# Kernel optimization log

Hardware: AMD Instinct MI355X
Metric: run time of the kernel (lower is better)

Reference implementation:

```python
import jax, jax.numpy as jnp
import numpy as np

B, S, D, H = 1, 4096, 1024, 16
DH = D // H  # 64
SCALE = D ** 0.5  # original divides by input_dim**0.5, not head_dim**0.5


def setup_inputs() -> dict:
    key = jax.random.key(0)
    ks = jax.random.split(key, 11)
    s = lambda i, shape, sc=1.0: jax.random.normal(ks[i], shape, dtype=jnp.float32) * sc
    w_init = 1.0 / np.sqrt(D)
    return {
        "q": s(0, (B, S, D)),
        "k": s(1, (B, S, D)),
        "v": s(2, (B, S, D)),
        "Wq": s(3, (H, D, DH), w_init),
        "bq": jnp.zeros((H, DH), jnp.float32),
        "Wk": s(4, (H, D, DH), w_init),
        "bk": jnp.zeros((H, DH), jnp.float32),
        "Wv": s(5, (H, D, DH), w_init),
        "bv": jnp.zeros((H, DH), jnp.float32),
        "Wo": s(6, (D, D), w_init),
        "bo": jnp.zeros((D,), jnp.float32),
    }


def reference(q, k, v, Wq, bq, Wk, bk, Wv, bv, Wo, bo):
    # Per-head Dense projections, batched over heads: [B,S,D] x [H,D,dh] -> [B,H,S,dh]
    Q = jnp.einsum("bsd,hde->bhse", q, Wq) + bq[None, :, None, :]
    K = jnp.einsum("bsd,hde->bhse", k, Wk) + bk[None, :, None, :]
    V = jnp.einsum("bsd,hde->bhse", v, Wv) + bv[None, :, None, :]
    # Scaled dot-product attention; note scale = sqrt(input_dim) as in source
    scores = jnp.einsum("bhse,bhte->bhst", Q, K) / SCALE  # [B,H,S,S]
    attn = jax.nn.softmax(scores, axis=-1)
    out = jnp.einsum("bhst,bhte->bhse", attn, V)  # [B,H,S,dh]
    # Concat heads along feature dim (head order matches the Python loop)
    concat = out.transpose(0, 2, 1, 3).reshape(q.shape[0], q.shape[1], H * DH)
    return concat @ Wo + bo
```

## Files before the change

### kernel.cpp

```cpp
#include <hip/hip_runtime.h>
#include <hip/hip_bf16.h>

#define S_LEN 4096
#define D_MODEL 1024
#define NH 16
#define DHEAD 64
#define QSCALE 0.0450843293f

typedef __attribute__((ext_vector_type(8))) short short8;
typedef __attribute__((ext_vector_type(4))) float floatx4;

__device__ __forceinline__ unsigned short f2bf(float f) {
    unsigned int x = __float_as_uint(f);
    x += 0x7fffu + ((x >> 16) & 1u);
    return (unsigned short)(x >> 16);
}

__device__ __forceinline__ float exp2_fast(float x) {
    return __builtin_amdgcn_exp2f(x);
}

__device__ __forceinline__ void async_copy16(const unsigned short* g, unsigned short* l) {
    __builtin_amdgcn_global_load_lds(
        (const __attribute__((address_space(1))) void*)g,
        (__attribute__((address_space(3))) void*)l, 16, 0, 0);
}

__global__ __launch_bounds__(256) void prep_all(
    const float* __restrict__ q, const float* __restrict__ k,
    const float* __restrict__ v,
    const float* __restrict__ Wq, const float* __restrict__ Wk,
    const float* __restrict__ Wv, const float* __restrict__ Wo,
    unsigned short* __restrict__ dst, unsigned short* __restrict__ ws)
{
    __shared__ float L[64][65];
    const int tid = threadIdx.x;

    if (blockIdx.x < 6144) {
        long i = (long)(blockIdx.x * 256 + tid) * 8;
        int which = (int)(i >> 22);
        long off = i & ((1 << 22) - 1);
        const float* src = (which == 0) ? q : (which == 1) ? k : v;
        float4 f0 = *(const float4*)&src[off];
        float4 f1 = *(const float4*)&src[off + 4];
        uint4 o;
        o.x = (unsigned int)f2bf(f0.x) | ((unsigned int)f2bf(f0.y) << 16);
        o.y = (unsigned int)f2bf(f0.z) | ((unsigned int)f2bf(f0.w) << 16);
        o.z = (unsigned int)f2bf(f1.x) | ((unsigned int)f2bf(f1.y) << 16);
        o.w = (unsigned int)f2bf(f1.z) | ((unsigned int)f2bf(f1.w) << 16);
        *(uint4*)&dst[i] = o;
        return;
    }

    const int bx  = blockIdx.x - 6144;
    const int mat = bx >> 8;

    if (mat < 3) {
        const float* W = (mat == 0) ? Wq : (mat == 1) ? Wk : Wv;
        unsigned short* WT = ws + (size_t)mat * (1u << 20);
        int h  = (bx >> 4) & 15;
        int dt = bx & 15;
        #pragma unroll
        for (int i = 0; i < 16; i++) {
            int idx = i * 256 + tid;
            int dp = idx >> 6, e = idx & 63;
            L[e][dp] = W[h * 65536 + (dt * 64 + dp) * 64 + e];
        }
        __syncthreads();
        #pragma unroll
        for (int i = 0; i < 16; i++) {
            int idx = i * 256 + tid;
            int e = idx >> 6, dp = idx & 63;
            WT[(h * 64 + e) * 1024 + dt * 64 + dp] = f2bf(L[e][dp]);
        }
    } else {
        unsigned short* WoT = ws + (size_t)3 * (1u << 20);
        int rt = (bx >> 4) & 15;
        int ct = bx & 15;
        #pragma unroll
        for (int i = 0; i < 16; i++) {
            int idx = i * 256 + tid;
            int dp = idx >> 6, np = idx & 63;
            L[np][dp] = Wo[(rt * 64 + dp) * 1024 + ct * 64 + np];
        }
        __syncthreads();
        #pragma unroll
        for (int i = 0; i < 16; i++) {
            int idx = i * 256 + tid;
            int np = idx >> 6, dp = idx & 63;
            WoT[(ct * 64 + np) * 1024 + rt * 64 + dp] = f2bf(L[np][dp]);
        }
    }
}

#define GEMM_CORE(XPTR, WPTR)                                                   \
    _Pragma("unroll")                                                           \
    for (int i = 0; i < 4; i++) {                                               \
        async_copy16(&XPTR[(size_t)(m0 + srow + i * 8) * D_MODEL + scol],       \
                     &LB[(wave * 32 + i * 8) * 64]);                            \
        async_copy16(&WPTR[(size_t)(n0 + srow + i * 8) * D_MODEL + scol],       \
                     &LB[16384 + (wave * 32 + i * 8) * 64]);                    \
    }                                                                           \
    asm volatile("s_waitcnt vmcnt(0)" ::: "memory");                            \
    __builtin_amdgcn_s_barrier();                                               \
    for (int k0 = 0; k0 < D_MODEL; k0 += 64) {                                  \
        const int cb = (k0 >> 6) & 1;                                           \
        const unsigned short* Ac = LB + cb * 8192;                              \
        const unsigned short* Bc = LB + 16384 + cb * 8192;                      \
        if (k0 + 64 < D_MODEL) {                                                \
            unsigned short* An = LB + (cb ^ 1) * 8192;                          \
            unsigned short* Bn = LB + 16384 + (cb ^ 1) * 8192;                  \
            _Pragma("unroll")                                                   \
            for (int i = 0; i < 4; i++) {                                       \
                async_copy16(&XPTR[(size_t)(m0 + srow + i * 8) * D_MODEL + k0 + 64 + scol], \
                             &An[(wave * 32 + i * 8) * 64]);                    \
                async_copy16(&WPTR[(size_t)(n0 + srow + i * 8) * D_MODEL + k0 + 64 + scol], \
                             &Bn[(wave * 32 + i * 8) * 64]);                    \
            }                                                                   \
        }                                                                       \
        _Pragma("unroll")                                                       \
        for (int ks = 0; ks < 2; ks++) {                                        \
            short8 af[4], bf[4];                                                \
            _Pragma("unroll")                                                   \
            for (int i = 0; i < 4; i++)                                         \
                af[i] = *(const short8*)&Ac[(wr * 64 + i * 16 + m) * 64 + ks * 32 + quad * 8]; \
            _Pragma("unroll")                                                   \
            for (int j = 0; j < 4; j++)                                         \
                bf[j] = *(const short8*)&Bc[(wc * 64 + j * 16 + m) * 64 + ks * 32 + quad * 8]; \
            __builtin_amdgcn_s_setprio(1);                                      \
            _Pragma("unroll")                                                   \
            for (int i = 0; i < 4; i++) {                                       \
                _Pragma("unroll")                                               \
                for (int j = 0; j < 4; j++)                                     \
                    acc[i][j] = __builtin_amdgcn_mfma_f32_16x16x32_bf16(af[i], bf[j], acc[i][j], 0, 0, 0); \
            }                                                                   \
            __builtin_amdgcn_s_setprio(0);                                      \
        }                                                                       \
        asm volatile("s_waitcnt vmcnt(0)" ::: "memory");                        \
        __builtin_amdgcn_s_barrier();                                           \
    }

__global__ __launch_bounds__(256) void qkv_gemm(
    const unsigned short* __restrict__ Xbase, const unsigned short* __restrict__ WTbase,
    const float* __restrict__ bq, const float* __restrict__ bk,
    const float* __restrict__ bv,
    unsigned short* __restrict__ Qbuf, unsigned short* __restrict__ Kbuf,
    unsigned short* __restrict__ Vbuf)
{
    __shared__ __align__(16) unsigned short LB[32768];

    const int z = blockIdx.z;
    const unsigned short* X  = Xbase + (size_t)z * (4u << 20);
    const unsigned short* WT = WTbase + (size_t)z * (1u << 20);
    const float* bias = (z == 0) ? bq : (z == 1) ? bk : bv;

    const int n0 = blockIdx.x * 128;
    const int m0 = blockIdx.y * 128;
    const int tid = threadIdx.x, wave = tid >> 6, lane = tid & 63;
    const int m = lane & 15, quad = lane >> 4;
    const int wr = wave >> 1, wc = wave & 1;
    const int srow = wave * 32 + (lane >> 3);
    const int scol = (lane & 7) * 8;

    floatx4 acc[4][4];
    #pragma unroll
    for (int i = 0; i < 4; i++)
        #pragma unroll
        for (int j = 0; j < 4; j++) acc[i][j] = (floatx4){0.f, 0.f, 0.f, 0.f};

    GEMM_CORE(X, WT)

    if (z == 2) {
        #pragma unroll
        for (int j = 0; j < 4; j++) {
            int n = n0 + wc * 64 + j * 16 + m;
            int h = n >> 6, e = n & 63;
            float bvv = bias[n];
            #pragma unroll
            for (int i = 0; i < 4; i++) {
                int sbase = m0 + wr * 64 + i * 16 + quad * 4;
                ushort4 pk;
                pk.x = f2bf(acc[i][j][0] + bvv);
                pk.y = f2bf(acc[i][j][1] + bvv);
                pk.z = f2bf(acc[i][j][2] + bvv);
                pk.w = f2bf(acc[i][j][3] + bvv);
                *(ushort4*)&Vbuf[h * (DHEAD * S_LEN) + e * S_LEN + sbase] = pk;
            }
        }
        return;
    }

    const float scale = (z == 0) ? QSCALE : 1.0f;
    unsigned short* outp = (z == 0) ? Qbuf : Kbuf;
    __syncthreads();
    unsigned short* stage = LB + (wc ? 8192 : 0);
    #pragma unroll
    for (int j = 0; j < 4; j++) {
        int e = j * 16 + m;
        float bvv = bias[n0 + wc * 64 + e];
        #pragma unroll
        for (int i = 0; i < 4; i++) {
            int rbase = wr * 64 + i * 16 + quad * 4;
            #pragma unroll
            for (int r = 0; r < 4; r++) {
                int rowl = rbase + r;
                stage[rowl * 64 + (e ^ ((rowl & 7) << 3))] =
                    f2bf((acc[i][j][r] + bvv) * scale);
            }
        }
    }
    __syncthreads();
    const int h0 = n0 >> 6;
    const size_t base0 = (size_t)h0 * (S_LEN * DHEAD) + (size_t)m0 * DHEAD;
    const size_t base1 = base0 + (size_t)(S_LEN * DHEAD);
    #pragma unroll
    for (int s = 0; s < 4; s++) {
        int o = tid * 8 + s * 2048;
        int row = o >> 6, c0 = o & 63;
        int cs = c0 ^ ((row & 7) << 3);
        *(uint4*)&outp[base0 + o] = *(const uint4*)&LB[row * 64 + cs];
        *(uint4*)&outp[base1 + o] = *(const uint4*)&LB[8192 + row * 64 + cs];
    }
}

__global__ __launch_bounds__(256) void out_gemm(
    const unsigned short* __restrict__ Cbuf, const unsigned short* __restrict__ WoT,
    const float* __restrict__ bo, float* __restrict__ out)
{
    __shared__ __align__(16) unsigned short LB[32768];

    const int n0 = blockIdx.x * 128;
    const int m0 = blockIdx.y * 128;
    const int tid = threadIdx.x, wave = tid >> 6, lane = tid & 63;
    const int m = lane & 15, quad = lane >> 4;
    const int wr = wave >> 1, wc = wave & 1;
    const int srow = wave * 32 + (lane >> 3);
    const int scol = (lane & 7) * 8;

    floatx4 acc[4][4];
    #pragma unroll
    for (int i = 0; i < 4; i++)
        #pragma unroll
        for (int j = 0; j < 4; j++) acc[i][j] = (floatx4){0.f, 0.f, 0.f, 0.f};

    GEMM_CORE(Cbuf, WoT)

    __syncthreads();
    float* Fs = (float*)LB;
    #pragma unroll
    for (int half = 0; half < 2; half++) {
        if (wr == half) {
            #pragma unroll
            for (int j = 0; j < 4; j++) {
                int c = wc * 64 + j * 16 + m;
                float bvv = bo[n0 + c];
                #pragma unroll
                for (int i = 0; i < 4; i++) {
                    int rbase = i * 16 + quad * 4;
                    #pragma unroll
                    for (int r = 0; r < 4; r++) {
                        int rowl = rbase + r;
                        Fs[rowl * 128 + (c ^ ((rowl & 7) << 2))] = acc[i][j][r] + bvv;
                    }
                }
            }
        }
        __syncthreads();
        #pragma unroll
        for (int s = 0; s < 8; s++) {
            int o = tid * 4 + s * 1024;
            int row = o >> 7, c0 = o & 127;
            int cs = c0 ^ ((row & 7) << 2);
            *(float4*)&out[(size_t)(m0 + half * 64 + row) * D_MODEL + n0 + c0] =
                *(const float4*)&Fs[row * 128 + cs];
        }
        __syncthreads();
    }
}

__global__ __launch_bounds__(512) void attn_kernel(
    const unsigned short* __restrict__ Q, const unsigned short* __restrict__ K,
    const unsigned short* __restrict__ VT, unsigned short* __restrict__ concat)
{
    __shared__ __align__(16) unsigned char ldsraw[65536];
    unsigned short* lds16 = (unsigned short*)ldsraw;

    const int h  = blockIdx.y;
    const int q0 = blockIdx.x * 256;
    const unsigned short* Qh = Q  + h * (S_LEN * DHEAD);
    const unsigned short* Kh = K  + h * (S_LEN * DHEAD);
    const unsigned short* Vh = VT + h * (DHEAD * S_LEN);

    const int tid  = threadIdx.x;
    const int wave = tid >> 6;
    const int wt   = wave & 3;
    const int wq2  = wave >> 2;
    const int lane = tid & 63;
    const int m    = lane & 15;
    const int quad = lane >> 4;
    const int swz  = (m & 7) << 3;
    const int lrow = lane >> 3;
    const int lcol = ((lane & 7) * 8) ^ (lrow << 3);

    unsigned short* Ps = lds16 + 16384;

    #pragma unroll
    for (int i = 0; i < 4; i++) {
        int c = 4 * wave + i;
        async_copy16(&Qh[(size_t)(q0 + 8 * c + lrow) * DHEAD + lcol], Ps + c * 512);
    }
    async_copy16(&Kh[(size_t)(8 * wave + lrow) * DHEAD + lcol], lds16 + wave * 512);
    async_copy16(&Vh[(size_t)(8 * wave + lrow) * S_LEN + lcol], lds16 + 8192 + wave * 512);
    asm volatile("s_waitcnt vmcnt(0)" ::: "memory");
    __builtin_amdgcn_s_barrier();

    short8 bq[8][2];
    #pragma unroll
    for (int qc = 0; qc < 8; qc++)
        #pragma unroll
        for (int ks = 0; ks < 2; ks++)
            bq[qc][ks] = *(const short8*)&Ps[(wq2 * 128 + qc * 16 + m) * 64 + ((ks * 32 + quad * 8) ^ swz)];
    __syncthreads();

    short8 vone;
    #pragma unroll
    for (int i = 0; i < 8; i++) vone[i] = (short)0x3F80;

    floatx4 O[2][4];
    #pragma unroll
    for (int mi = 0; mi < 2; mi++)
        #pragma unroll
        for (int nb = 0; nb < 4; nb++) O[mi][nb] = (floatx4){0.f, 0.f, 0.f, 0.f};
    floatx4 Lacc[2];
    Lacc[0] = (floatx4){0.f, 0.f, 0.f, 0.f};
    Lacc[1] = (floatx4){0.f, 0.f, 0.f, 0.f};

    for (int t0 = 0; t0 < S_LEN; t0 += 64) {
        const int cur = (t0 >> 6) & 1;
        unsigned short* Ksc = lds16 + cur * 4096;
        unsigned short* Vsc = lds16 + 8192 + cur * 4096;

        if (t0) {
            asm volatile("s_waitcnt vmcnt(0)" ::: "memory");
            __builtin_amdgcn_s_barrier();
        }
        if (t0 + 64 < S_LEN) {
            unsigned short* Ksn = lds16 + (cur ^ 1) * 4096;
            unsigned short* Vsn = lds16 + 8192 + (cur ^ 1) * 4096;
            async_copy16(&Kh[(size_t)(t0 + 64 + 8 * wave + lrow) * DHEAD + lcol],
                         Ksn + wave * 512);
            async_copy16(&Vh[(size_t)(8 * wave + lrow) * S_LEN + t0 + 64 + lcol],
                         Vsn + wave * 512);
        }

        floatx4 st[8];
        #pragma unroll
        for (int qc = 0; qc < 8; qc++) st[qc] = (floatx4){0.f, 0.f, 0.f, 0.f};
        #pragma unroll
        for (int ks = 0; ks < 2; ks++) {
            short8 a = *(const short8*)&Ksc[(wt * 16 + m) * 64 + ((ks * 32 + quad * 8) ^ swz)];
            __builtin_amdgcn_s_setprio(1);
            #pragma unroll
            for (int qc = 0; qc < 8; qc++)
                st[qc] = __builtin_amdgcn_mfma_f32_16x16x32_bf16(a, bq[qc][ks], st[qc], 0, 0, 0);
            __builtin_amdgcn_s_setprio(0);
        }

        #pragma unroll
        for (int qc = 0; qc < 8; qc++) {
            float p0 = exp2_fast(st[qc][0]);
            float p1 = exp2_fast(st[qc][1]);
            float p2 = exp2_fast(st[qc][2]);
            float p3 = exp2_fast(st[qc][3]);
            unsigned r0, r1;
            asm("v_cvt_pk_bf16_f32 %0, %1, %2" : "=v"(r0) : "v"(p0), "v"(p1));
            asm("v_cvt_pk_bf16_f32 %0, %1, %2" : "=v"(r1) : "v"(p2), "v"(p3));
            uint2 pk;
            pk.x = r0;
            pk.y = r1;
            *(uint2*)&Ps[(wq2 * 128 + qc * 16 + m) * 64 + ((wt * 16 + quad * 4) ^ swz)] = pk;
        }
        asm volatile("s_waitcnt lgkmcnt(0)" ::: "memory");
        __builtin_amdgcn_s_barrier();

        #pragma unroll
        for (int ks = 0; ks < 2; ks++) {
            short8 ap0 = *(const short8*)&Ps[(wave * 32 + m) * 64 + ((ks * 32 + quad * 8) ^ swz)];
            short8 ap1 = *(const short8*)&Ps[(wave * 32 + 16 + m) * 64 + ((ks * 32 + quad * 8) ^ swz)];
            __builtin_amdgcn_s_setprio(1);
            #pragma unroll
            for (int nb = 0; nb < 4; nb++) {
                short8 bv = *(const short8*)&Vsc[(nb * 16 + m) * 64 + ((ks * 32 + quad * 8) ^ swz)];
                O[0][nb] = __builtin_amdgcn_mfma_f32_16x16x32_bf16(ap0, bv, O[0][nb], 0, 0, 0);
                O[1][nb] = __builtin_amdgcn_mfma_f32_16x16x32_bf16(ap1, bv, O[1][nb], 0, 0, 0);
            }
            Lacc[0] = __builtin_amdgcn_mfma_f32_16x16x32_bf16(ap0, vone, Lacc[0], 0, 0, 0);
            Lacc[1] = __builtin_amdgcn_mfma_f32_16x16x32_bf16(ap1, vone, Lacc[1], 0, 0, 0);
            __builtin_amdgcn_s_setprio(0);
        }
    }

    #pragma unroll
    for (int mi = 0; mi < 2; mi++) {
        float linv[4];
        #pragma unroll
        for (int r = 0; r < 4; r++) linv[r] = 1.0f / Lacc[mi][r];
        #pragma unroll
        for (int nb = 0; nb < 4; nb++) {
            int e = nb * 16 + m;
            #pragma unroll
            for (int r = 0; r < 4; r++) {
                int s = q0 + wave * 32 + mi * 16 + quad * 4 + r;
                concat[s * D_MODEL + h * DHEAD + e] = f2bf(O[mi][nb][r] * linv[r]);
            }
        }
    }
}

extern "C" void kernel_launch(void* const* d_in, const int* in_sizes, int n_in,
                              void* d_out, int out_size, void* d_ws, size_t ws_size,
                              hipStream_t stream) {
    const float* q  = (const float*)d_in[0];
    const float* k  = (const float*)d_in[1];
    const float* v  = (const float*)d_in[2];
    const float* Wq = (const float*)d_in[3];
    const float* bq = (const float*)d_in[4];
    const float* Wk = (const float*)d_in[5];
    const float* bk = (const float*)d_in[6];
    const float* Wv = (const float*)d_in[7];
    const float* bv = (const float*)d_in[8];
    const float* Wo = (const float*)d_in[9];
    const float* bo = (const float*)d_in[10];
    float* out = (float*)d_out;

    unsigned short* ws = (unsigned short*)d_ws;
    const size_t M1 = 1u << 20;
    unsigned short* WqT  = ws;
    unsigned short* WoT  = ws + 3 * M1;
    unsigned short* Qbuf = ws + 4 * M1;
    unsigned short* Kbuf = ws + 8 * M1;
    unsigned short* Vbuf = ws + 12 * M1;
    unsigned short* Cbuf = ws + 16 * M1;
    unsigned short* qb   = ws + 20 * M1;

    prep_all<<<7168, 256, 0, stream>>>(q, k, v, Wq, Wk, Wv, Wo, qb, ws);

    dim3 gq(8, 32, 3);
    qkv_gemm<<<gq, 256, 0, stream>>>(qb, WqT, bq, bk, bv, Qbuf, Kbuf, Vbuf);

    dim3 ga(16, 16);
    attn_kernel<<<ga, 512, 0, stream>>>(Qbuf, Kbuf, Vbuf, Cbuf);

    dim3 gg(8, 32);
    out_gemm<<<gg, 256, 0, stream>>>(Cbuf, WoT, bo, out);
}
```

Measured before the change: 258.8 us.

## Software-pipeline attention with a 4-deep K/V ring, overlapping QK with the previous tile's softmax and PV

```diff
diff --git a/kernel.cpp b/kernel.cpp
--- a/kernel.cpp
+++ b/kernel.cpp
@@ -278,11 +278,81 @@
     }
 }
 
+#define ATTN_STQK(CUR, KIDX)                                                    \
+    do {                                                                        \
+        const unsigned short* Ksc = lds16 + (KIDX) * 4096;                      \
+        _Pragma("unroll")                                                       \
+        for (int qc = 0; qc < 8; qc++) CUR[qc] = (floatx4){0.f, 0.f, 0.f, 0.f}; \
+        _Pragma("unroll")                                                       \
+        for (int ks = 0; ks < 2; ks++) {                                        \
+            short8 a = *(const short8*)&Ksc[(wt * 16 + m) * 64 + ((ks * 32 + quad * 8) ^ swz)]; \
+            __builtin_amdgcn_s_setprio(1);                                      \
+            _Pragma("unroll")                                                   \
+            for (int qc = 0; qc < 8; qc++)                                      \
+                CUR[qc] = __builtin_amdgcn_mfma_f32_16x16x32_bf16(a, bq[qc][ks], CUR[qc], 0, 0, 0); \
+            __builtin_amdgcn_s_setprio(0);                                      \
+        }                                                                       \
+    } while (0)
+
+#define ATTN_SOFTMAX(PREV)                                                      \
+    do {                                                                        \
+        _Pragma("unroll")                                                       \
+        for (int qc = 0; qc < 8; qc++) {                                        \
+            float p0 = exp2_fast(PREV[qc][0]);                                  \
+            float p1 = exp2_fast(PREV[qc][1]);                                  \
+            float p2 = exp2_fast(PREV[qc][2]);                                  \
+            float p3 = exp2_fast(PREV[qc][3]);                                  \
+            unsigned r0, r1;                                                    \
+            asm("v_cvt_pk_bf16_f32 %0, %1, %2" : "=v"(r0) : "v"(p0), "v"(p1));  \
+            asm("v_cvt_pk_bf16_f32 %0, %1, %2" : "=v"(r1) : "v"(p2), "v"(p3));  \
+            uint2 pk; pk.x = r0; pk.y = r1;                                     \
+            *(uint2*)&Ps[(wq2 * 128 + qc * 16 + m) * 64 + ((wt * 16 + quad * 4) ^ swz)] = pk; \
+        }                                                                       \
+    } while (0)
+
+#define ATTN_PV(VIDX)                                                           \
+    do {                                                                        \
+        const unsigned short* Vsc = lds16 + 16384 + (VIDX) * 4096;              \
+        _Pragma("unroll")                                                       \
+        for (int ks = 0; ks < 2; ks++) {                                        \
+            short8 ap0 = *(const short8*)&Ps[(wave * 32 + m) * 64 + ((ks * 32 + quad * 8) ^ swz)]; \
+            short8 ap1 = *(const short8*)&Ps[(wave * 32 + 16 + m) * 64 + ((ks * 32 + quad * 8) ^ swz)]; \
+            __builtin_amdgcn_s_setprio(1);                                      \
+            _Pragma("unroll")                                                   \
+            for (int nb = 0; nb < 4; nb++) {                                    \
+                short8 bv = *(const short8*)&Vsc[(nb * 16 + m) * 64 + ((ks * 32 + quad * 8) ^ swz)]; \
+                O[0][nb] = __builtin_amdgcn_mfma_f32_16x16x32_bf16(ap0, bv, O[0][nb], 0, 0, 0); \
+                O[1][nb] = __builtin_amdgcn_mfma_f32_16x16x32_bf16(ap1, bv, O[1][nb], 0, 0, 0); \
+            }                                                                   \
+            Lacc[0] = __builtin_amdgcn_mfma_f32_16x16x32_bf16(ap0, vone, Lacc[0], 0, 0, 0); \
+            Lacc[1] = __builtin_amdgcn_mfma_f32_16x16x32_bf16(ap1, vone, Lacc[1], 0, 0, 0); \
+            __builtin_amdgcn_s_setprio(0);                                      \
+        }                                                                       \
+    } while (0)
+
+#define ATTN_BODY(I, CUR, PREV, VMSTR)                                          \
+    do {                                                                        \
+        asm volatile("s_waitcnt " VMSTR ::: "memory");                          \
+        __builtin_amdgcn_s_barrier();                                           \
+        if ((I) + 2 < 64) {                                                     \
+            int tb = ((I) + 2) & 3;                                             \
+            async_copy16(&Kh[(size_t)(((I) + 2) * 64 + 8 * wave + lrow) * DHEAD + lcol], \
+                         lds16 + tb * 4096 + wave * 512);                       \
+            async_copy16(&Vh[(size_t)(8 * wave + lrow) * S_LEN + ((I) + 2) * 64 + lcol], \
+                         lds16 + 16384 + tb * 4096 + wave * 512);               \
+        }                                                                       \
+        ATTN_STQK(CUR, (I) & 3);                                                \
+        ATTN_SOFTMAX(PREV);                                                     \
+        asm volatile("s_waitcnt lgkmcnt(0)" ::: "memory");                      \
+        __builtin_amdgcn_s_barrier();                                           \
+        ATTN_PV(((I) - 1) & 3);                                                 \
+    } while (0)
+
 __global__ __launch_bounds__(512) void attn_kernel(
     const unsigned short* __restrict__ Q, const unsigned short* __restrict__ K,
     const unsigned short* __restrict__ VT, unsigned short* __restrict__ concat)
 {
-    __shared__ __align__(16) unsigned char ldsraw[65536];
+    __shared__ __align__(16) unsigned char ldsraw[98304];
     unsigned short* lds16 = (unsigned short*)ldsraw;
 
     const int h  = blockIdx.y;
@@ -302,7 +372,7 @@
     const int lrow = lane >> 3;
     const int lcol = ((lane & 7) * 8) ^ (lrow << 3);
 
-    unsigned short* Ps = lds16 + 16384;
+    unsigned short* Ps = lds16 + 32768;
 
     #pragma unroll
     for (int i = 0; i < 4; i++) {
@@ -310,7 +380,7 @@
         async_copy16(&Qh[(size_t)(q0 + 8 * c + lrow) * DHEAD + lcol], Ps + c * 512);
     }
     async_copy16(&Kh[(size_t)(8 * wave + lrow) * DHEAD + lcol], lds16 + wave * 512);
-    async_copy16(&Vh[(size_t)(8 * wave + lrow) * S_LEN + lcol], lds16 + 8192 + wave * 512);
+    async_copy16(&Vh[(size_t)(8 * wave + lrow) * S_LEN + lcol], lds16 + 16384 + wave * 512);
     asm volatile("s_waitcnt vmcnt(0)" ::: "memory");
     __builtin_amdgcn_s_barrier();
 
@@ -321,6 +391,11 @@
         for (int ks = 0; ks < 2; ks++)
             bq[qc][ks] = *(const short8*)&Ps[(wq2 * 128 + qc * 16 + m) * 64 + ((ks * 32 + quad * 8) ^ swz)];
     __syncthreads();
+
+    async_copy16(&Kh[(size_t)(64 + 8 * wave + lrow) * DHEAD + lcol], lds16 + 4096 + wave * 512);
+    async_copy16(&Vh[(size_t)(8 * wave + lrow) * S_LEN + 64 + lcol], lds16 + 16384 + 4096 + wave * 512);
+    async_copy16(&Kh[(size_t)(128 + 8 * wave + lrow) * DHEAD + lcol], lds16 + 2 * 4096 + wave * 512);
+    async_copy16(&Vh[(size_t)(8 * wave + lrow) * S_LEN + 128 + lcol], lds16 + 16384 + 2 * 4096 + wave * 512);
 
     short8 vone;
     #pragma unroll
@@ -335,70 +410,19 @@
     Lacc[0] = (floatx4){0.f, 0.f, 0.f, 0.f};
     Lacc[1] = (floatx4){0.f, 0.f, 0.f, 0.f};
 
-    for (int t0 = 0; t0 < S_LEN; t0 += 64) {
-        const int cur = (t0 >> 6) & 1;
-        unsigned short* Ksc = lds16 + cur * 4096;
-        unsigned short* Vsc = lds16 + 8192 + cur * 4096;
-
-        if (t0) {
-            asm volatile("s_waitcnt vmcnt(0)" ::: "memory");
-            __builtin_amdgcn_s_barrier();
-        }
-        if (t0 + 64 < S_LEN) {
-            unsigned short* Ksn = lds16 + (cur ^ 1) * 4096;
-            unsigned short* Vsn = lds16 + 8192 + (cur ^ 1) * 4096;
-            async_copy16(&Kh[(size_t)(t0 + 64 + 8 * wave + lrow) * DHEAD + lcol],
-                         Ksn + wave * 512);
-            async_copy16(&Vh[(size_t)(8 * wave + lrow) * S_LEN + t0 + 64 + lcol],
-                         Vsn + wave * 512);
-        }
-
-        floatx4 st[8];
-        #pragma unroll
-        for (int qc = 0; qc < 8; qc++) st[qc] = (floatx4){0.f, 0.f, 0.f, 0.f};
-        #pragma unroll
-        for (int ks = 0; ks < 2; ks++) {
-            short8 a = *(const short8*)&Ksc[(wt * 16 + m) * 64 + ((ks * 32 + quad * 8) ^ swz)];
-            __builtin_amdgcn_s_setprio(1);
-            #pragma unroll
-            for (int qc = 0; qc < 8; qc++)
-                st[qc] = __builtin_amdgcn_mfma_f32_16x16x32_bf16(a, bq[qc][ks], st[qc], 0, 0, 0);
-            __builtin_amdgcn_s_setprio(0);
-        }
-
-        #pragma unroll
-        for (int qc = 0; qc < 8; qc++) {
-            float p0 = exp2_fast(st[qc][0]);
-            float p1 = exp2_fast(st[qc][1]);
-            float p2 = exp2_fast(st[qc][2]);
-            float p3 = exp2_fast(st[qc][3]);
-            unsigned r0, r1;
-            asm("v_cvt_pk_bf16_f32 %0, %1, %2" : "=v"(r0) : "v"(p0), "v"(p1));
-            asm("v_cvt_pk_bf16_f32 %0, %1, %2" : "=v"(r1) : "v"(p2), "v"(p3));
-            uint2 pk;
-            pk.x = r0;
-            pk.y = r1;
-            *(uint2*)&Ps[(wq2 * 128 + qc * 16 + m) * 64 + ((wt * 16 + quad * 4) ^ swz)] = pk;
-        }
-        asm volatile("s_waitcnt lgkmcnt(0)" ::: "memory");
-        __builtin_amdgcn_s_barrier();
-
-        #pragma unroll
-        for (int ks = 0; ks < 2; ks++) {
-            short8 ap0 = *(const short8*)&Ps[(wave * 32 + m) * 64 + ((ks * 32 + quad * 8) ^ swz)];
-            short8 ap1 = *(const short8*)&Ps[(wave * 32 + 16 + m) * 64 + ((ks * 32 + quad * 8) ^ swz)];
-            __builtin_amdgcn_s_setprio(1);
-            #pragma unroll
-            for (int nb = 0; nb < 4; nb++) {
-                short8 bv = *(const short8*)&Vsc[(nb * 16 + m) * 64 + ((ks * 32 + quad * 8) ^ swz)];
-                O[0][nb] = __builtin_amdgcn_mfma_f32_16x16x32_bf16(ap0, bv, O[0][nb], 0, 0, 0);
-                O[1][nb] = __builtin_amdgcn_mfma_f32_16x16x32_bf16(ap1, bv, O[1][nb], 0, 0, 0);
-            }
-            Lacc[0] = __builtin_amdgcn_mfma_f32_16x16x32_bf16(ap0, vone, Lacc[0], 0, 0, 0);
-            Lacc[1] = __builtin_amdgcn_mfma_f32_16x16x32_bf16(ap1, vone, Lacc[1], 0, 0, 0);
-            __builtin_amdgcn_s_setprio(0);
-        }
-    }
+    floatx4 stA[8], stB[8];
+    ATTN_STQK(stA, 0);
+
+    for (int ii = 1; ii < 62; ii += 2) {
+        ATTN_BODY(ii,     stB, stA, "vmcnt(2)");
+        ATTN_BODY(ii + 1, stA, stB, "vmcnt(2)");
+    }
+    ATTN_BODY(63, stB, stA, "vmcnt(0)");
+
+    ATTN_SOFTMAX(stB);
+    asm volatile("s_waitcnt lgkmcnt(0)" ::: "memory");
+    __builtin_amdgcn_s_barrier();
+    ATTN_PV(3);
 
     #pragma unroll
     for (int mi = 0; mi < 2; mi++) {
```

After: 264.0 us. 1.02x slower.

## Fuse fp32-to-bf16 activation conversion into QKV GEMM and swizzle LDS tiles

Applied to the files above, without the earlier changes.

```diff
diff --git a/kernel.cpp b/kernel.cpp
--- a/kernel.cpp
+++ b/kernel.cpp
@@ -26,34 +26,15 @@
         (__attribute__((address_space(3))) void*)l, 16, 0, 0);
 }
 
-__global__ __launch_bounds__(256) void prep_all(
-    const float* __restrict__ q, const float* __restrict__ k,
-    const float* __restrict__ v,
+__global__ __launch_bounds__(256) void prep_w(
     const float* __restrict__ Wq, const float* __restrict__ Wk,
     const float* __restrict__ Wv, const float* __restrict__ Wo,
-    unsigned short* __restrict__ dst, unsigned short* __restrict__ ws)
+    unsigned short* __restrict__ ws)
 {
     __shared__ float L[64][65];
+    const int bx  = blockIdx.x;
+    const int mat = bx >> 8;
     const int tid = threadIdx.x;
-
-    if (blockIdx.x < 6144) {
-        long i = (long)(blockIdx.x * 256 + tid) * 8;
-        int which = (int)(i >> 22);
-        long off = i & ((1 << 22) - 1);
-        const float* src = (which == 0) ? q : (which == 1) ? k : v;
-        float4 f0 = *(const float4*)&src[off];
-        float4 f1 = *(const float4*)&src[off + 4];
-        uint4 o;
-        o.x = (unsigned int)f2bf(f0.x) | ((unsigned int)f2bf(f0.y) << 16);
-        o.y = (unsigned int)f2bf(f0.z) | ((unsigned int)f2bf(f0.w) << 16);
-        o.z = (unsigned int)f2bf(f1.x) | ((unsigned int)f2bf(f1.y) << 16);
-        o.w = (unsigned int)f2bf(f1.z) | ((unsigned int)f2bf(f1.w) << 16);
-        *(uint4*)&dst[i] = o;
-        return;
-    }
-
-    const int bx  = blockIdx.x - 6144;
-    const int mat = bx >> 8;
 
     if (mat < 3) {
         const float* W = (mat == 0) ? Wq : (mat == 1) ? Wk : Wv;
@@ -93,12 +74,12 @@
     }
 }
 
-#define GEMM_CORE(XPTR, WPTR)                                                   \
+#define GEMM_CORE2(XPTR, WPTR)                                                  \
     _Pragma("unroll")                                                           \
     for (int i = 0; i < 4; i++) {                                               \
-        async_copy16(&XPTR[(size_t)(m0 + srow + i * 8) * D_MODEL + scol],       \
+        async_copy16(&XPTR[(size_t)(m0 + wave * 32 + i * 8 + lrow) * D_MODEL + lcol], \
                      &LB[(wave * 32 + i * 8) * 64]);                            \
-        async_copy16(&WPTR[(size_t)(n0 + srow + i * 8) * D_MODEL + scol],       \
+        async_copy16(&WPTR[(size_t)(n0 + wave * 32 + i * 8 + lrow) * D_MODEL + lcol], \
                      &LB[16384 + (wave * 32 + i * 8) * 64]);                    \
     }                                                                           \
     asm volatile("s_waitcnt vmcnt(0)" ::: "memory");                            \
@@ -112,9 +93,9 @@
             unsigned short* Bn = LB + 16384 + (cb ^ 1) * 8192;                  \
             _Pragma("unroll")                                                   \
             for (int i = 0; i < 4; i++) {                                       \
-                async_copy16(&XPTR[(size_t)(m0 + srow + i * 8) * D_MODEL + k0 + 64 + scol], \
+                async_copy16(&XPTR[(size_t)(m0 + wave * 32 + i * 8 + lrow) * D_MODEL + k0 + 64 + lcol], \
                              &An[(wave * 32 + i * 8) * 64]);                    \
-                async_copy16(&WPTR[(size_t)(n0 + srow + i * 8) * D_MODEL + k0 + 64 + scol], \
+                async_copy16(&WPTR[(size_t)(n0 + wave * 32 + i * 8 + lrow) * D_MODEL + k0 + 64 + lcol], \
                              &Bn[(wave * 32 + i * 8) * 64]);                    \
             }                                                                   \
         }                                                                       \
@@ -123,10 +104,10 @@
             short8 af[4], bf[4];                                                \
             _Pragma("unroll")                                                   \
             for (int i = 0; i < 4; i++)                                         \
-                af[i] = *(const short8*)&Ac[(wr * 64 + i * 16 + m) * 64 + ks * 32 + quad * 8]; \
+                af[i] = *(const short8*)&Ac[(wr * 64 + i * 16 + m) * 64 + ((ks * 32 + quad * 8) ^ rsw)]; \
             _Pragma("unroll")                                                   \
             for (int j = 0; j < 4; j++)                                         \
-                bf[j] = *(const short8*)&Bc[(wc * 64 + j * 16 + m) * 64 + ks * 32 + quad * 8]; \
+                bf[j] = *(const short8*)&Bc[(wc * 64 + j * 16 + m) * 64 + ((ks * 32 + quad * 8) ^ rsw)]; \
             __builtin_amdgcn_s_setprio(1);                                      \
             _Pragma("unroll")                                                   \
             for (int i = 0; i < 4; i++) {                                       \
@@ -136,12 +117,15 @@
             }                                                                   \
             __builtin_amdgcn_s_setprio(0);                                      \
         }                                                                       \
-        asm volatile("s_waitcnt vmcnt(0)" ::: "memory");                        \
-        __builtin_amdgcn_s_barrier();                                           \
+        if (k0 + 64 < D_MODEL) {                                                \
+            asm volatile("s_waitcnt vmcnt(0)" ::: "memory");                    \
+            __builtin_amdgcn_s_barrier();                                       \
+        }                                                                       \
     }
 
 __global__ __launch_bounds__(256) void qkv_gemm(
-    const unsigned short* __restrict__ Xbase, const unsigned short* __restrict__ WTbase,
+    const float* __restrict__ qin, const float* __restrict__ kin,
+    const float* __restrict__ vin, const unsigned short* __restrict__ WTbase,
     const float* __restrict__ bq, const float* __restrict__ bk,
     const float* __restrict__ bv,
     unsigned short* __restrict__ Qbuf, unsigned short* __restrict__ Kbuf,
@@ -150,7 +134,7 @@
     __shared__ __align__(16) unsigned short LB[32768];
 
     const int z = blockIdx.z;
-    const unsigned short* X  = Xbase + (size_t)z * (4u << 20);
+    const float* X = (z == 0) ? qin : (z == 1) ? kin : vin;
     const unsigned short* WT = WTbase + (size_t)z * (1u << 20);
     const float* bias = (z == 0) ? bq : (z == 1) ? bk : bv;
 
@@ -159,8 +143,9 @@
     const int tid = threadIdx.x, wave = tid >> 6, lane = tid & 63;
     const int m = lane & 15, quad = lane >> 4;
     const int wr = wave >> 1, wc = wave & 1;
-    const int srow = wave * 32 + (lane >> 3);
-    const int scol = (lane & 7) * 8;
+    const int lrow = lane >> 3;
+    const int lcol = ((lane & 7) * 8) ^ (lrow << 3);
+    const int rsw  = (m & 7) << 3;
 
     floatx4 acc[4][4];
     #pragma unroll
@@ -168,7 +153,77 @@
         #pragma unroll
         for (int j = 0; j < 4; j++) acc[i][j] = (floatx4){0.f, 0.f, 0.f, 0.f};
 
-    GEMM_CORE(X, WT)
+    float4 a0[4], a1[4];
+    #pragma unroll
+    for (int i = 0; i < 4; i++) {
+        const float* src = &X[(size_t)(m0 + wave * 32 + i * 8 + lrow) * D_MODEL + (lane & 7) * 8];
+        a0[i] = *(const float4*)src;
+        a1[i] = *(const float4*)(src + 4);
+        async_copy16(&WT[(size_t)(n0 + wave * 32 + i * 8 + lrow) * D_MODEL + lcol],
+                     &LB[16384 + (wave * 32 + i * 8) * 64]);
+    }
+    #pragma unroll
+    for (int i = 0; i < 4; i++) {
+        unsigned u0, u1, u2, u3;
+        asm("v_cvt_pk_bf16_f32 %0, %1, %2" : "=v"(u0) : "v"(a0[i].x), "v"(a0[i].y));
+        asm("v_cvt_pk_bf16_f32 %0, %1, %2" : "=v"(u1) : "v"(a0[i].z), "v"(a0[i].w));
+        asm("v_cvt_pk_bf16_f32 %0, %1, %2" : "=v"(u2) : "v"(a1[i].x), "v"(a1[i].y));
+        asm("v_cvt_pk_bf16_f32 %0, %1, %2" : "=v"(u3) : "v"(a1[i].z), "v"(a1[i].w));
+        uint4 w4; w4.x = u0; w4.y = u1; w4.z = u2; w4.w = u3;
+        *(uint4*)&LB[(wave * 32 + i * 8 + lrow) * 64 + lcol] = w4;
+    }
+    asm volatile("s_waitcnt vmcnt(0) lgkmcnt(0)" ::: "memory");
+    __builtin_amdgcn_s_barrier();
+
+    for (int k0 = 0; k0 < D_MODEL; k0 += 64) {
+        const int cb = (k0 >> 6) & 1;
+        const unsigned short* Ac = LB + cb * 8192;
+        const unsigned short* Bc = LB + 16384 + cb * 8192;
+        const bool more = (k0 + 64 < D_MODEL);
+        if (more) {
+            #pragma unroll
+            for (int i = 0; i < 4; i++) {
+                const float* src = &X[(size_t)(m0 + wave * 32 + i * 8 + lrow) * D_MODEL + k0 + 64 + (lane & 7) * 8];
+                a0[i] = *(const float4*)src;
+                a1[i] = *(const float4*)(src + 4);
+                async_copy16(&WT[(size_t)(n0 + wave * 32 + i * 8 + lrow) * D_MODEL + k0 + 64 + lcol],
+                             &LB[16384 + (cb ^ 1) * 8192 + (wave * 32 + i * 8) * 64]);
+            }
+        }
+        #pragma unroll
+        for (int ks = 0; ks < 2; ks++) {
+            short8 af[4], bf[4];
+            #pragma unroll
+            for (int i = 0; i < 4; i++)
+                af[i] = *(const short8*)&Ac[(wr * 64 + i * 16 + m) * 64 + ((ks * 32 + quad * 8) ^ rsw)];
+            #pragma unroll
+            for (int j = 0; j < 4; j++)
+                bf[j] = *(const short8*)&Bc[(wc * 64 + j * 16 + m) * 64 + ((ks * 32 + quad * 8) ^ rsw)];
+            __builtin_amdgcn_s_setprio(1);
+            #pragma unroll
+            for (int i = 0; i < 4; i++) {
+                #pragma unroll
+                for (int j = 0; j < 4; j++)
+                    acc[i][j] = __builtin_amdgcn_mfma_f32_16x16x32_bf16(af[i], bf[j], acc[i][j], 0, 0, 0);
+            }
+            __builtin_amdgcn_s_setprio(0);
+        }
+        if (more) {
+            unsigned short* An = LB + (cb ^ 1) * 8192;
+            #pragma unroll
+            for (int i = 0; i < 4; i++) {
+                unsigned u0, u1, u2, u3;
+                asm("v_cvt_pk_bf16_f32 %0, %1, %2" : "=v"(u0) : "v"(a0[i].x), "v"(a0[i].y));
+                asm("v_cvt_pk_bf16_f32 %0, %1, %2" : "=v"(u1) : "v"(a0[i].z), "v"(a0[i].w));
+                asm("v_cvt_pk_bf16_f32 %0, %1, %2" : "=v"(u2) : "v"(a1[i].x), "v"(a1[i].y));
+                asm("v_cvt_pk_bf16_f32 %0, %1, %2" : "=v"(u3) : "v"(a1[i].z), "v"(a1[i].w));
+                uint4 w4; w4.x = u0; w4.y = u1; w4.z = u2; w4.w = u3;
+                *(uint4*)&An[(wave * 32 + i * 8 + lrow) * 64 + lcol] = w4;
+            }
+            asm volatile("s_waitcnt vmcnt(0) lgkmcnt(0)" ::: "memory");
+            __builtin_amdgcn_s_barrier();
+        }
+    }
 
     if (z == 2) {
         #pragma unroll
@@ -234,8 +289,9 @@
     const int tid = threadIdx.x, wave = tid >> 6, lane = tid & 63;
     const int m = lane & 15, quad = lane >> 4;
     const int wr = wave >> 1, wc = wave & 1;
-    const int srow = wave * 32 + (lane >> 3);
-    const int scol = (lane & 7) * 8;
+    const int lrow = lane >> 3;
+    const int lcol = ((lane & 7) * 8) ^ (lrow << 3);
+    const int rsw  = (m & 7) << 3;
 
     floatx4 acc[4][4];
     #pragma unroll
@@ -243,7 +299,7 @@
         #pragma unroll
         for (int j = 0; j < 4; j++) acc[i][j] = (floatx4){0.f, 0.f, 0.f, 0.f};
 
-    GEMM_CORE(Cbuf, WoT)
+    GEMM_CORE2(Cbuf, WoT)
 
     __syncthreads();
     float* Fs = (float*)LB;
@@ -441,12 +497,11 @@
     unsigned short* Kbuf = ws + 8 * M1;
     unsigned short* Vbuf = ws + 12 * M1;
     unsigned short* Cbuf = ws + 16 * M1;
-    unsigned short* qb   = ws + 20 * M1;
-
-    prep_all<<<7168, 256, 0, stream>>>(q, k, v, Wq, Wk, Wv, Wo, qb, ws);
+
+    prep_w<<<1024, 256, 0, stream>>>(Wq, Wk, Wv, Wo, ws);
 
     dim3 gq(8, 32, 3);
-    qkv_gemm<<<gq, 256, 0, stream>>>(qb, WqT, bq, bk, bv, Qbuf, Kbuf, Vbuf);
+    qkv_gemm<<<gq, 256, 0, stream>>>(q, k, v, WqT, bq, bk, bv, Qbuf, Kbuf, Vbuf);
 
     dim3 ga(16, 16);
     attn_kernel<<<ga, 512, 0, stream>>>(Qbuf, Kbuf, Vbuf, Cbuf);
```

Result: slower. 273.2 us (+5.6%).
